# Kernel tuning notes

Hardware: AMD Instinct MI355X
Metric: run time of the kernel (lower is better)

The kernel has to match this reference:

```python
import jax, jax.numpy as jnp
import numpy as np

DIM = 1536; HEADS = 12; HD = DIM // HEADS; FFN = 8960; EPS = 1e-6; T5 = 512
B = 1; F_ = 8; H_ = 18; W_ = 24; S = F_ * H_ * W_; L2 = T5 + 257


def _ln(x, w=None, b=None):
    m = x.mean(-1, keepdims=True)
    v = ((x - m) ** 2).mean(-1, keepdims=True)
    y = (x - m) * jax.lax.rsqrt(v + EPS)
    return y * w + b if w is not None else y


def _rms(x, w):
    return x * jax.lax.rsqrt(jnp.mean(x * x, -1, keepdims=True) + EPS) * w


def _gelu_tanh(z):
    return 0.5 * z * (1.0 + jnp.tanh(0.7978845608028654 * (z + 0.044715 * z * z * z)))


def _rope(x, F, H, W, ang):
    # x: [B,S,n,d]; ang: [1024, d//2] rotation angles (axial 3D RoPE)
    b, s, n, d = x.shape
    c = d // 2
    c1 = c // 3; c0 = c - 2 * c1  # split sizes [c0, c1, c1] over (F,H,W)
    fa = jnp.broadcast_to(ang[:F, :c0][:, None, None, :], (F, H, W, c0))
    ha = jnp.broadcast_to(ang[:H, c0:c0 + c1][None, :, None, :], (F, H, W, c1))
    wa = jnp.broadcast_to(ang[:W, c0 + c1:][None, None, :, :], (F, H, W, c1))
    th = jnp.concatenate([fa, ha, wa], -1).reshape(1, s, 1, c)
    cs, sn = jnp.cos(th), jnp.sin(th)
    xr = x.reshape(b, s, n, c, 2)
    re, im = xr[..., 0], xr[..., 1]
    return jnp.stack([re * cs - im * sn, re * sn + im * cs], -1).reshape(b, s, n, d)


def _attn(q, k, v):
    # dense softmax attention; [B,Lq,n,d] x [B,Lk,n,d]
    s = jnp.einsum('bqnd,bknd->bnqk', q, k) * (1.0 / np.sqrt(q.shape[-1]))
    p = jax.nn.softmax(s, axis=-1)
    return jnp.einsum('bnqk,bknd->bqnd', p, v)


def setup_inputs() -> dict:
    key = jax.random.key(0)
    ks = iter(jax.random.split(key, 64))
    g = lambda shp, sc=0.02: jax.random.normal(next(ks), shp, dtype=jnp.float32) * sc
    inp = {
        'x': jax.random.normal(next(ks), (B, S, DIM), dtype=jnp.float32),
        'e': jax.random.normal(next(ks), (B, 6, DIM), dtype=jnp.float32),
        'context': jax.random.normal(next(ks), (B, L2, DIM), dtype=jnp.float32),
        'freqs': jax.random.uniform(next(ks), (1024, HD // 2), dtype=jnp.float32),
        'modulation': g((1, 6, DIM)),
        'sa_qw': g((DIM, DIM)), 'sa_qb': jnp.zeros((DIM,), jnp.float32),
        'sa_kw': g((DIM, DIM)), 'sa_kb': jnp.zeros((DIM,), jnp.float32),
        'sa_vw': g((DIM, DIM)), 'sa_vb': jnp.zeros((DIM,), jnp.float32),
        'sa_ow': g((DIM, DIM)), 'sa_ob': jnp.zeros((DIM,), jnp.float32),
        'sa_nq': jnp.ones((DIM,), jnp.float32), 'sa_nk': jnp.ones((DIM,), jnp.float32),
        'norm3_w': jnp.ones((DIM,), jnp.float32), 'norm3_b': jnp.zeros((DIM,), jnp.float32),
        'ca_qw': g((DIM, DIM)), 'ca_qb': jnp.zeros((DIM,), jnp.float32),
        'ca_kw': g((DIM, DIM)), 'ca_kb': jnp.zeros((DIM,), jnp.float32),
        'ca_vw': g((DIM, DIM)), 'ca_vb': jnp.zeros((DIM,), jnp.float32),
        'ca_kiw': g((DIM, DIM)), 'ca_kib': jnp.zeros((DIM,), jnp.float32),
        'ca_viw': g((DIM, DIM)), 'ca_vib': jnp.zeros((DIM,), jnp.float32),
        'ca_ow': g((DIM, DIM)), 'ca_ob': jnp.zeros((DIM,), jnp.float32),
        'ca_nq': jnp.ones((DIM,), jnp.float32), 'ca_nk': jnp.ones((DIM,), jnp.float32),
        'ca_nki': jnp.ones((DIM,), jnp.float32),
        'ffn_w1': g((DIM, FFN)), 'ffn_b1': jnp.zeros((FFN,), jnp.float32),
        'ffn_w2': g((FFN, DIM)), 'ffn_b2': jnp.zeros((DIM,), jnp.float32),
        'F': F_, 'H': H_, 'W': W_,
    }
    return inp


def reference(x, e, context, freqs, modulation, sa_qw, sa_qb, sa_kw, sa_kb, sa_vw, sa_vb,
              sa_ow, sa_ob, sa_nq, sa_nk, norm3_w, norm3_b, ca_qw, ca_qb, ca_kw, ca_kb,
              ca_vw, ca_vb, ca_kiw, ca_kib, ca_viw, ca_vib, ca_ow, ca_ob, ca_nq, ca_nk,
              ca_nki, ffn_w1, ffn_b1, ffn_w2, ffn_b2, F, H, W):
    b, s, c = x.shape
    e6 = modulation + e                    # [B,6,C]
    e0, e1, e2, e3, e4, e5 = [e6[:, i:i + 1] for i in range(6)]

    # ---- self attention (with 3D RoPE, qk RMSNorm) ----
    xs = _ln(x) * (1.0 + e1) + e0
    q = _rms(xs @ sa_qw + sa_qb, sa_nq).reshape(b, s, HEADS, HD)
    k = _rms(xs @ sa_kw + sa_kb, sa_nk).reshape(b, s, HEADS, HD)
    v = (xs @ sa_vw + sa_vb).reshape(b, s, HEADS, HD)
    q = _rope(q, F, H, W, freqs)
    k = _rope(k, F, H, W, freqs)
    y = _attn(q, k, v).reshape(b, s, c) @ sa_ow + sa_ob
    x = x + y * e2

    # ---- i2v cross attention: text tokens (last T5) + image tokens (first L2-T5) ----
    xc = _ln(x, norm3_w, norm3_b)
    img_len = context.shape[1] - T5
    ctx_img = context[:, :img_len]
    ctx_txt = context[:, img_len:]
    q = _rms(xc @ ca_qw + ca_qb, ca_nq).reshape(b, s, HEADS, HD)
    k = _rms(ctx_txt @ ca_kw + ca_kb, ca_nk).reshape(b, T5, HEADS, HD)
    v = (ctx_txt @ ca_vw + ca_vb).reshape(b, T5, HEADS, HD)
    ki = _rms(ctx_img @ ca_kiw + ca_kib, ca_nki).reshape(b, img_len, HEADS, HD)
    vi = (ctx_img @ ca_viw + ca_vib).reshape(b, img_len, HEADS, HD)
    a = _attn(q, k, v) + _attn(q, ki, vi)
    x = x + a.reshape(b, s, c) @ ca_ow + ca_ob

    # ---- FFN with adaLN modulation ----
    z = _ln(x) * (1.0 + e4) + e3
    y = _gelu_tanh(z @ ffn_w1 + ffn_b1) @ ffn_w2 + ffn_b2
    x = x + y * e5
    return x
```

## Files before the change

kernel.cpp:

```cpp
#include <hip/hip_runtime.h>
#include <stdint.h>

#define DIM 1536
#define NHEADS 12
#define HD 128
#define FFN 8960
#define SQ 3456
#define T5 512
#define LCTX 769
#define IMG 257
#define IMGP 384
#define EPSL 1e-6f

typedef __bf16 bf16;
typedef __bf16 bf16x8 __attribute__((ext_vector_type(8)));
typedef float f32x4 __attribute__((ext_vector_type(4)));

__device__ inline bf16x8 zero_bf16x8() {
  bf16x8 v;
  for (int i = 0; i < 8; i++) v[i] = (bf16)0.0f;
  return v;
}

__device__ inline void glds16(const bf16* g, bf16* lds) {
  __builtin_amdgcn_global_load_lds(
      (const __attribute__((address_space(1))) void*)g,
      (__attribute__((address_space(3))) void*)lds, 16, 0, 0);
}

__device__ inline bf16x8 rot8(bf16x8 v, int r) {
  union U { bf16x8 b; uint32_t d[4]; };
  U u; u.b = v;
  uint32_t e0 = (r & 4) ? u.d[2] : u.d[0], e1 = (r & 4) ? u.d[3] : u.d[1];
  uint32_t e2 = (r & 4) ? u.d[0] : u.d[2], e3 = (r & 4) ? u.d[1] : u.d[3];
  uint32_t f0 = (r & 2) ? e1 : e0, f1 = (r & 2) ? e2 : e1;
  uint32_t f2 = (r & 2) ? e3 : e2, f3 = (r & 2) ? e0 : e3;
  U o;
  o.d[0] = (r & 1) ? __builtin_amdgcn_alignbit(f1, f0, 16) : f0;
  o.d[1] = (r & 1) ? __builtin_amdgcn_alignbit(f2, f1, 16) : f1;
  o.d[2] = (r & 1) ? __builtin_amdgcn_alignbit(f3, f2, 16) : f2;
  o.d[3] = (r & 1) ? __builtin_amdgcn_alignbit(f0, f3, 16) : f3;
  return o.b;
}


__global__ void prep_small_kernel(const float* __restrict__ modv, const float* __restrict__ e,
                                  float* __restrict__ e6f,
                                  const float* __restrict__ qb, const float* __restrict__ kb,
                                  const float* __restrict__ vb, float* __restrict__ qkvB,
                                  const float* __restrict__ ckb, const float* __restrict__ cvb,
                                  float* __restrict__ kvB,
                                  const float* __restrict__ kib, const float* __restrict__ vib,
                                  float* __restrict__ kivB) {
  int i = blockIdx.x * 256 + threadIdx.x;
  if (i < 6 * DIM) e6f[i] = modv[i] + e[i];
  if (i < DIM) {
    qkvB[i] = qb[i]; qkvB[i + DIM] = kb[i]; qkvB[i + 2 * DIM] = vb[i];
    kvB[i] = ckb[i]; kvB[i + DIM] = cvb[i];
    kivB[i] = kib[i]; kivB[i + DIM] = vib[i];
  }
}

__global__ void prep_ctx_kernel(const float* __restrict__ ctx, bf16* __restrict__ ctxt,
                                bf16* __restrict__ ctxi) {
  int i = blockIdx.x * 256 + threadIdx.x;
  if (i < T5 * DIM) ctxt[i] = (bf16)ctx[(size_t)IMG * DIM + i];
  if (i < IMGP * DIM) {
    int r = i / DIM;
    ctxi[i] = (r < IMG) ? (bf16)ctx[i] : (bf16)0.0f;
  }
}

__global__ void transpose_w3_kernel(const float* __restrict__ W0, const float* __restrict__ W1,
                                    const float* __restrict__ W2, bf16* __restrict__ Wt,
                                    int K, int N) {
  __shared__ float tile[32][33];
  const float* W = blockIdx.z == 0 ? W0 : (blockIdx.z == 1 ? W1 : W2);
  bf16* dst = Wt + (size_t)blockIdx.z * K * N;
  int n0 = blockIdx.x * 32, k0 = blockIdx.y * 32;
  int tx = threadIdx.x, ty = threadIdx.y;
  for (int i = ty; i < 32; i += 8)
    tile[i][tx] = W[(size_t)(k0 + i) * N + n0 + tx];
  __syncthreads();
  for (int i = ty; i < 32; i += 8)
    dst[(size_t)(n0 + i) * K + k0 + tx] = (bf16)tile[tx][i];
}

__device__ inline void block_reduce2(float& s1, float& s2) {
  __shared__ float buf[8];
  for (int off = 32; off; off >>= 1) {
    s1 += __shfl_down(s1, off, 64);
    s2 += __shfl_down(s2, off, 64);
  }
  int w = threadIdx.x >> 6;
  if ((threadIdx.x & 63) == 0) { buf[w] = s1; buf[w + 4] = s2; }
  __syncthreads();
  s1 = buf[0] + buf[1] + buf[2] + buf[3];
  s2 = buf[4] + buf[5] + buf[6] + buf[7];
  __syncthreads();
}

__global__ __launch_bounds__(256) void ln_mod_kernel(
    const float* __restrict__ X, const float* __restrict__ gamma,
    const float* __restrict__ beta, int plus_one, bf16* __restrict__ out) {
  int r = blockIdx.x;
  const float* xr = X + (size_t)r * DIM;
  float v[6], s = 0.f, s2 = 0.f;
  for (int i = 0; i < 6; i++) {
    v[i] = xr[threadIdx.x + i * 256];
    s += v[i]; s2 += v[i] * v[i];
  }
  block_reduce2(s, s2);
  float mean = s * (1.0f / DIM);
  float var = s2 * (1.0f / DIM) - mean * mean;
  float rstd = rsqrtf(var + EPSL);
  float add1 = plus_one ? 1.0f : 0.0f;
  for (int i = 0; i < 6; i++) {
    int c = threadIdx.x + i * 256;
    out[(size_t)r * DIM + c] = (bf16)(((v[i] - mean) * rstd) * (gamma[c] + add1) + beta[c]);
  }
}

__global__ __launch_bounds__(256) void rms_rope_multi_kernel(
    const float* __restrict__ X, int istride, int nsec,
    const float* __restrict__ nw0, const float* __restrict__ nw1,
    int mode0, int mode1, int mode2,
    const float* __restrict__ freqs,
    bf16* __restrict__ o0, bf16* __restrict__ o1, bf16* __restrict__ o2) {
  int sec = blockIdx.y;
  int r = blockIdx.x;
  const float* xr = X + (size_t)r * istride + sec * DIM;
  const float* nw = sec == 0 ? nw0 : nw1;
  bf16* out = (sec == 0 ? o0 : (sec == 1 ? o1 : o2)) + (size_t)r * DIM;
  int mode = sec == 0 ? mode0 : (sec == 1 ? mode1 : mode2);
  float v[6];
  for (int i = 0; i < 6; i++) v[i] = xr[threadIdx.x + i * 256];
  if (mode == 0) {
    for (int i = 0; i < 6; i++) out[threadIdx.x + i * 256] = (bf16)v[i];
    return;
  }
  float s2 = 0.f, dummy = 0.f;
  for (int i = 0; i < 6; i++) s2 += v[i] * v[i];
  block_reduce2(s2, dummy);
  float rms = rsqrtf(s2 * (1.0f / DIM) + EPSL);
  if (mode == 1) {
    for (int i = 0; i < 6; i++) {
      int c = threadIdx.x + i * 256;
      out[c] = (bf16)(v[i] * rms * nw[c]);
    }
  } else {
    int f = r / (18 * 24), rem = r % (18 * 24), hh = rem / 24, ww = rem % 24;
    for (int i = 0; i < 3; i++) {
      int p = threadIdx.x + i * 256;
      int id = p & 63;
      int idx = id < 22 ? f : (id < 43 ? hh : ww);
      float th = freqs[idx * 64 + id];
      float cs = __cosf(th), sn = __sinf(th);
      float re = xr[2 * p] * rms * nw[2 * p];
      float im = xr[2 * p + 1] * rms * nw[2 * p + 1];
      out[2 * p]     = (bf16)(re * cs - im * sn);
      out[2 * p + 1] = (bf16)(re * sn + im * cs);
    }
  }
}

__global__ void ffn2_reduce_kernel(const float* __restrict__ p, const float* __restrict__ b2,
                                   const float* __restrict__ e5, const float* __restrict__ xcur,
                                   float* __restrict__ out) {
  int i = blockIdx.x * 256 + threadIdx.x;
  if (i >= SQ * DIM) return;
  int col = i % DIM;
  out[i] = xcur[i] + (p[i] + p[i + (size_t)SQ * DIM] + b2[col]) * e5[col];
}

template <int BM>
__global__ __launch_bounds__(256) void gemm_db_kernel(
    const bf16* __restrict__ A, const bf16* __restrict__ Wt,
    const float* __restrict__ bias, const float* __restrict__ scalev,
    const float* __restrict__ resid, float* __restrict__ outF,
    bf16* __restrict__ outB, int M, int N, int K, int gelu, int ksplit) {
  constexpr int MI = BM / 32;
  constexpr int NAW = BM / 64;
  __shared__ bf16 As[2][BM * 32];
  __shared__ bf16 Bs[2][128 * 32];
  int tid = threadIdx.x;
  int tm0 = blockIdx.y * BM, tn0 = blockIdx.x * 128;
  int lane = tid & 63, wave = tid >> 6;
  int quad = lane >> 4, l16 = lane & 15;
  int mbase = (wave >> 1) * (BM / 2), nbase = (wave & 1) * 64;
  int lrow = lane >> 2, lcol = (lane & 3) * 8;
  int klen = K / ksplit;
  int kbeg = blockIdx.z * klen;

  const bf16* aP[NAW];
  const bf16* bP[2];
#pragma unroll
  for (int j = 0; j < NAW; j++) {
    int c = wave * NAW + j;
    aP[j] = A + (size_t)(tm0 + c * 16 + lrow) * K + kbeg + lcol;
  }
#pragma unroll
  for (int j = 0; j < 2; j++) {
    int c = wave * 2 + j;
    bP[j] = Wt + (size_t)(tn0 + c * 16 + lrow) * K + kbeg + lcol;
  }

  f32x4 acc[MI][4];
#pragma unroll
  for (int mi = 0; mi < MI; mi++)
    for (int ni = 0; ni < 4; ni++)
      for (int rr = 0; rr < 4; rr++) acc[mi][ni][rr] = 0.0f;

  auto stage = [&](int buf) {
#pragma unroll
    for (int j = 0; j < NAW; j++) {
      glds16(aP[j], &As[buf][(wave * NAW + j) * 512]);
      aP[j] += 32;
    }
#pragma unroll
    for (int j = 0; j < 2; j++) {
      glds16(bP[j], &Bs[buf][(wave * 2 + j) * 512]);
      bP[j] += 32;
    }
  };

  int niter = klen / 32;
  stage(0);
  int cur = 0;
  for (int it = 0; it < niter; it++) {
    __syncthreads();
    if (it + 1 < niter) stage(cur ^ 1);
    bf16x8 af[MI], bfr[4];
#pragma unroll
    for (int mi = 0; mi < MI; mi++)
      af[mi] = *(bf16x8*)&As[cur][(mbase + mi * 16 + l16) * 32 + quad * 8];
#pragma unroll
    for (int ni = 0; ni < 4; ni++)
      bfr[ni] = *(bf16x8*)&Bs[cur][(nbase + ni * 16 + l16) * 32 + quad * 8];
#pragma unroll
    for (int mi = 0; mi < MI; mi++)
#pragma unroll
      for (int ni = 0; ni < 4; ni++)
        acc[mi][ni] = __builtin_amdgcn_mfma_f32_16x16x32_bf16(af[mi], bfr[ni], acc[mi][ni], 0, 0, 0);
    cur ^= 1;
  }

  if (ksplit > 1) {
    float* po = outF + (size_t)blockIdx.z * M * N;
#pragma unroll
    for (int mi = 0; mi < MI; mi++) {
      int rbase = tm0 + mbase + mi * 16 + quad * 4;
#pragma unroll
      for (int ni = 0; ni < 4; ni++) {
        int col = tn0 + nbase + ni * 16 + l16;
        for (int rr = 0; rr < 4; rr++)
          po[(size_t)(rbase + rr) * N + col] = acc[mi][ni][rr];
      }
    }
    return;
  }

#pragma unroll
  for (int mi = 0; mi < MI; mi++) {
    int rbase = tm0 + mbase + mi * 16 + quad * 4;
#pragma unroll
    for (int ni = 0; ni < 4; ni++) {
      int col = tn0 + nbase + ni * 16 + l16;
      float b = bias ? bias[col] : 0.0f;
      float sc = scalev ? scalev[col] : 1.0f;
      for (int rr = 0; rr < 4; rr++) {
        int row = rbase + rr;
        float t = acc[mi][ni][rr] + b;
        if (gelu) {
          float z = t;
          float u = 0.7978845608028654f * (z + 0.044715f * z * z * z);
          t = z / (1.0f + __expf(-2.0f * u));
        }
        t *= sc;
        size_t idx = (size_t)row * N + col;
        if (resid) t += resid[idx];
        if (outF) outF[idx] = t;
        else outB[idx] = (bf16)t;
      }
    }
  }
}

__global__ __launch_bounds__(256) void attn_kernel(
    const bf16* __restrict__ Q, const bf16* __restrict__ Kb, const bf16* __restrict__ Vb,
    float* __restrict__ Opart, float* __restrict__ mlb,
    int L, int kchunk, int zoff) {
  __shared__ bf16 Ks[64][136];
  __shared__ bf16 Vts[128][72];
  __shared__ bf16 Ps[4][16][72];

  int nwg = gridDim.x * gridDim.y * gridDim.z;
  int flat = blockIdx.x + gridDim.x * (blockIdx.y + gridDim.y * blockIdx.z);
  if ((nwg & 7) == 0) flat = (flat & 7) * (nwg >> 3) + (flat >> 3);
  int bx = flat % gridDim.x;
  int rest = flat / gridDim.x;
  int hb = rest % gridDim.y;
  int bz = rest / gridDim.y;

  int tid = threadIdx.x;
  int q0 = bx * 64;
  int zabs = zoff + bz;
  int kbeg = bz * kchunk;
  int kend = min(L, kbeg + kchunk);
  int klen = kend - kbeg;
  int lane = tid & 63, wave = tid >> 6;
  int quad = lane >> 4, l16 = lane & 15;
  int qrow = q0 + wave * 16 + l16;

  bf16x8 qf[4];
#pragma unroll
  for (int c = 0; c < 4; c++)
    qf[c] = *(const bf16x8*)(Q + (size_t)qrow * DIM + hb * HD + c * 32 + quad * 8);

  bf16x8 onesv;
#pragma unroll
  for (int i = 0; i < 8; i++) onesv[i] = (bf16)1.0f;

  f32x4 o[8];
#pragma unroll
  for (int ff = 0; ff < 8; ff++)
    for (int rr = 0; rr < 4; rr++) o[ff][rr] = 0.0f;
  float m_i[4], l_i[4];
#pragma unroll
  for (int r = 0; r < 4; r++) { m_i[r] = -1e30f; l_i[r] = 0.0f; }
  const float sc = 0.08838834764831845f;

  int srow = tid >> 2, scolc = tid & 3;
  int rot = (2 * scolc + (srow & 1)) & 7;
  int nt = (klen + 63) / 64;

  const bf16* kp0 = Kb + (size_t)(kbeg + srow) * DIM + hb * HD + scolc * 8;
  const bf16* vp0 = Vb + (size_t)(kbeg + srow) * DIM + hb * HD + scolc * 8;

  bf16x8 kreg[4], vreg[4];
  if (srow < klen) {
#pragma unroll
    for (int c = 0; c < 4; c++) {
      kreg[c] = *(const bf16x8*)(kp0 + c * 32);
      vreg[c] = *(const bf16x8*)(vp0 + c * 32);
    }
  } else {
#pragma unroll
    for (int c = 0; c < 4; c++) { kreg[c] = zero_bf16x8(); vreg[c] = zero_bf16x8(); }
  }

  for (int kt = 0; kt < nt; kt++) {
    __syncthreads();
#pragma unroll
    for (int c = 0; c < 4; c++)
      *(bf16x8*)&Ks[srow][scolc * 8 + c * 32] = kreg[c];
#pragma unroll
    for (int c = 0; c < 4; c++) {
      bf16x8 rv = rot8(vreg[c], rot);
      int v0 = scolc * 8 + c * 32;
#pragma unroll
      for (int i = 0; i < 8; i++) {
        int jj = (i + rot) & 7;
        Vts[v0 + jj][srow] = rv[i];
      }
    }
    if (kt + 1 < nt) {
      int key = (kt + 1) * 64 + srow;
      const bf16* kp = kp0 + (size_t)(kt + 1) * 64 * DIM;
      const bf16* vp = vp0 + (size_t)(kt + 1) * 64 * DIM;
      if (key < klen) {
#pragma unroll
        for (int c = 0; c < 4; c++) {
          kreg[c] = *(const bf16x8*)(kp + c * 32);
          vreg[c] = *(const bf16x8*)(vp + c * 32);
        }
      } else {
#pragma unroll
        for (int c = 0; c < 4; c++) { kreg[c] = zero_bf16x8(); vreg[c] = zero_bf16x8(); }
      }
    }
    __syncthreads();

    f32x4 sfr[4];
    __builtin_amdgcn_s_setprio(1);
#pragma unroll
    for (int nf = 0; nf < 4; nf++) {
      f32x4 a;
      for (int rr = 0; rr < 4; rr++) a[rr] = 0.0f;
#pragma unroll
      for (int c = 0; c < 4; c++) {
        bf16x8 kf = *(bf16x8*)&Ks[nf * 16 + l16][c * 32 + quad * 8];
        a = __builtin_amdgcn_mfma_f32_16x16x32_bf16(qf[c], kf, a, 0, 0, 0);
      }
      sfr[nf] = a;
    }
    __builtin_amdgcn_s_setprio(0);

#pragma unroll
    for (int nf = 0; nf < 4; nf++) {
      int colg = kt * 64 + nf * 16 + l16;
      bool valid = colg < klen;
#pragma unroll
      for (int r = 0; r < 4; r++)
        sfr[nf][r] = valid ? sfr[nf][r] * sc : -1e30f;
    }

    float lmax[4];
#pragma unroll
    for (int r = 0; r < 4; r++)
      lmax[r] = fmaxf(fmaxf(sfr[0][r], sfr[1][r]), fmaxf(sfr[2][r], sfr[3][r]));
    int ok = (lmax[0] <= m_i[0] + 8.0f) & (lmax[1] <= m_i[1] + 8.0f) &
             (lmax[2] <= m_i[2] + 8.0f) & (lmax[3] <= m_i[3] + 8.0f);
    if (!__all(ok)) {
#pragma unroll
      for (int r = 0; r < 4; r++) {
        float t = lmax[r];
#pragma unroll
        for (int off = 1; off < 16; off <<= 1) t = fmaxf(t, __shfl_xor(t, off, 64));
        float mnew = fmaxf(m_i[r], t);
        float alpha = __expf(m_i[r] - mnew);
        m_i[r] = mnew;
        l_i[r] *= alpha;
#pragma unroll
        for (int ff = 0; ff < 8; ff++) o[ff][r] *= alpha;
      }
    }

#pragma unroll
    for (int r = 0; r < 4; r++) {
      char* prow = (char*)&Ps[wave][quad * 4 + r][0];
      int swzW = ((quad >> 1) & 1) << 5;
#pragma unroll
      for (int nf = 0; nf < 4; nf++) {
        float p = __expf(sfr[nf][r] - m_i[r]);
        *(bf16*)(prow + (((nf * 16 + l16) * 2) ^ swzW)) = (bf16)p;
      }
    }
    int swzR = ((l16 >> 3) & 1) << 5;
    bf16x8 pf[2];
#pragma unroll
    for (int ks = 0; ks < 2; ks++)
      pf[ks] = *(bf16x8*)((char*)&Ps[wave][l16][0] + (((ks * 32 + quad * 8) * 2) ^ swzR));

    __builtin_amdgcn_s_setprio(1);
    f32x4 ld;
    for (int rr = 0; rr < 4; rr++) ld[rr] = 0.0f;
    ld = __builtin_amdgcn_mfma_f32_16x16x32_bf16(pf[0], onesv, ld, 0, 0, 0);
    ld = __builtin_amdgcn_mfma_f32_16x16x32_bf16(pf[1], onesv, ld, 0, 0, 0);
#pragma unroll
    for (int ff = 0; ff < 8; ff++) {
#pragma unroll
      for (int ks = 0; ks < 2; ks++) {
        bf16x8 vf = *(bf16x8*)&Vts[ff * 16 + l16][ks * 32 + quad * 8];
        o[ff] = __builtin_amdgcn_mfma_f32_16x16x32_bf16(pf[ks], vf, o[ff], 0, 0, 0);
      }
    }
    __builtin_amdgcn_s_setprio(0);
#pragma unroll
    for (int r = 0; r < 4; r++) l_i[r] += ld[r];
  }

  float* po = Opart + (size_t)zabs * SQ * DIM;
#pragma unroll
  for (int r = 0; r < 4; r++) {
    float inv = 1.0f / l_i[r];
#pragma unroll
    for (int ff = 0; ff < 8; ff++) o[ff][r] *= inv;
  }
#pragma unroll
  for (int ff = 0; ff < 8; ff++) {
#pragma unroll
    for (int r = 0; r < 4; r++) {
      int row = q0 + wave * 16 + quad * 4 + r;
      int col = hb * HD + ff * 16 + l16;
      po[(size_t)row * DIM + col] = o[ff][r];
    }
  }
  if (l16 == 0) {
#pragma unroll
    for (int r = 0; r < 4; r++) {
      int row = q0 + wave * 16 + quad * 4 + r;
      size_t mi = (((size_t)zabs * NHEADS + hb) * SQ + row) * 2;
      mlb[mi] = m_i[r];
      mlb[mi + 1] = l_i[r];
    }
  }
}

__global__ __launch_bounds__(256) void attn_combine_kernel(
    const float* __restrict__ Op, const float* __restrict__ mlb,
    bf16* __restrict__ out, int nmerge, int addslot) {
  int row = blockIdx.x;
  __shared__ float wsh[3 * NHEADS];
  int t = threadIdx.x;
  if (t < NHEADS) {
    float m[3], l[3];
    for (int z = 0; z < 3; z++) {
      if (z < nmerge) {
        size_t b = (((size_t)z * NHEADS + t) * SQ + row) * 2;
        m[z] = mlb[b]; l[z] = mlb[b + 1];
      } else {
        m[z] = -1e30f; l[z] = 0.0f;
      }
    }
    float M = fmaxf(m[0], fmaxf(m[1], m[2]));
    float w0 = l[0] * __expf(m[0] - M);
    float w1 = l[1] * __expf(m[1] - M);
    float w2 = l[2] * __expf(m[2] - M);
    float inv = 1.0f / (w0 + w1 + w2);
    wsh[t] = w0 * inv;
    wsh[NHEADS + t] = w1 * inv;
    wsh[2 * NHEADS + t] = w2 * inv;
  }
  __syncthreads();
#pragma unroll
  for (int i = 0; i < 6; i++) {
    int c = t + i * 256;
    int h = c >> 7;
    float acc = wsh[h] * Op[((size_t)0 * SQ + row) * DIM + c];
    if (nmerge > 1) acc += wsh[NHEADS + h] * Op[((size_t)1 * SQ + row) * DIM + c];
    if (nmerge > 2) acc += wsh[2 * NHEADS + h] * Op[((size_t)2 * SQ + row) * DIM + c];
    if (addslot >= 0) acc += Op[((size_t)addslot * SQ + row) * DIM + c];
    out[(size_t)row * DIM + c] = (bf16)acc;
  }
}


extern "C" void kernel_launch(void* const* d_in, const int* in_sizes, int n_in,
                              void* d_out, int out_size, void* d_ws, size_t ws_size,
                              hipStream_t stream) {
  const float* x      = (const float*)d_in[0];
  const float* e      = (const float*)d_in[1];
  const float* ctx    = (const float*)d_in[2];
  const float* freqs  = (const float*)d_in[3];
  const float* modv   = (const float*)d_in[4];
  const float* sa_qw  = (const float*)d_in[5];
  const float* sa_qb  = (const float*)d_in[6];
  const float* sa_kw  = (const float*)d_in[7];
  const float* sa_kb  = (const float*)d_in[8];
  const float* sa_vw  = (const float*)d_in[9];
  const float* sa_vb  = (const float*)d_in[10];
  const float* sa_ow  = (const float*)d_in[11];
  const float* sa_ob  = (const float*)d_in[12];
  const float* sa_nq  = (const float*)d_in[13];
  const float* sa_nk  = (const float*)d_in[14];
  const float* norm3w = (const float*)d_in[15];
  const float* norm3b = (const float*)d_in[16];
  const float* ca_qw  = (const float*)d_in[17];
  const float* ca_qb  = (const float*)d_in[18];
  const float* ca_kw  = (const float*)d_in[19];
  const float* ca_kb  = (const float*)d_in[20];
  const float* ca_vw  = (const float*)d_in[21];
  const float* ca_vb  = (const float*)d_in[22];
  const float* ca_kiw = (const float*)d_in[23];
  const float* ca_kib = (const float*)d_in[24];
  const float* ca_viw = (const float*)d_in[25];
  const float* ca_vib = (const float*)d_in[26];
  const float* ca_ow  = (const float*)d_in[27];
  const float* ca_ob  = (const float*)d_in[28];
  const float* ca_nq  = (const float*)d_in[29];
  const float* ca_nk  = (const float*)d_in[30];
  const float* ca_nki = (const float*)d_in[31];
  const float* ffn_w1 = (const float*)d_in[32];
  const float* ffn_b1 = (const float*)d_in[33];
  const float* ffn_w2 = (const float*)d_in[34];
  const float* ffn_b2 = (const float*)d_in[35];

  char* ws = (char*)d_ws;
  size_t off = 0;
  auto alloc = [&](size_t bytes) -> void* {
    void* p = ws + off;
    off += (bytes + 255) & ~(size_t)255;
    return p;
  };
  float* e6f   = (float*)alloc((size_t)6 * DIM * 4);
  bf16* act_bf = (bf16*)alloc((size_t)SQ * DIM * 2);
  bf16* q_bf   = (bf16*)alloc((size_t)SQ * DIM * 2);
  bf16* k_bf   = (bf16*)alloc((size_t)SQ * DIM * 2);
  bf16* v_bf   = (bf16*)alloc((size_t)SQ * DIM * 2);
  char* big0   = (char*)alloc((size_t)SQ * 3 * DIM * 4);
  float* xcur  = (float*)alloc((size_t)SQ * DIM * 4);
  bf16* wbig   = (bf16*)alloc((size_t)FFN * DIM * 2);
  bf16* wsm    = (bf16*)alloc((size_t)3 * DIM * DIM * 2);
  bf16* ctxt_bf = (bf16*)alloc((size_t)T5 * DIM * 2);
  bf16* ctxi_bf = (bf16*)alloc((size_t)IMGP * DIM * 2);
  float* ctxkvF = (float*)alloc((size_t)T5 * 2 * DIM * 4);
  float* ctxkivF = (float*)alloc((size_t)IMGP * 2 * DIM * 4);
  bf16* kt_bf  = (bf16*)alloc((size_t)T5 * DIM * 2);
  bf16* vt_bf  = (bf16*)alloc((size_t)T5 * DIM * 2);
  bf16* ki_bf  = (bf16*)alloc((size_t)IMGP * DIM * 2);
  bf16* vi_bf  = (bf16*)alloc((size_t)IMGP * DIM * 2);
  float* qkvB  = (float*)alloc((size_t)3 * DIM * 4);
  float* kvB   = (float*)alloc((size_t)2 * DIM * 4);
  float* kivB  = (float*)alloc((size_t)2 * DIM * 4);
  float* mlbuf = (float*)alloc((size_t)3 * NHEADS * SQ * 2 * 4);

  float* qkvF = (float*)big0;
  float* projf = (float*)big0;
  float* opart = (float*)big0;
  bf16* y1 = (bf16*)big0;
  float* pbuf = (float*)act_bf;

  const float* e0 = e6f;
  const float* e1 = e6f + DIM;
  const float* e2 = e6f + 2 * DIM;
  const float* e3 = e6f + 3 * DIM;
  const float* e4 = e6f + 4 * DIM;
  const float* e5 = e6f + 5 * DIM;

  dim3 tblk(32, 8);

  prep_small_kernel<<<(6 * DIM + 255) / 256, 256, 0, stream>>>(
      modv, e, e6f, sa_qb, sa_kb, sa_vb, qkvB, ca_kb, ca_vb, kvB, ca_kib, ca_vib, kivB);

  ln_mod_kernel<<<SQ, 256, 0, stream>>>(x, e1, e0, 1, act_bf);

  transpose_w3_kernel<<<dim3(48, 48, 3), tblk, 0, stream>>>(sa_qw, sa_kw, sa_vw, wbig, DIM, DIM);
  gemm_db_kernel<128><<<dim3(3 * DIM / 128, SQ / 128), 256, 0, stream>>>(
      act_bf, wbig, qkvB, nullptr, nullptr, qkvF, nullptr, SQ, 3 * DIM, DIM, 0, 1);
  rms_rope_multi_kernel<<<dim3(SQ, 3), 256, 0, stream>>>(
      qkvF, 3 * DIM, 3, sa_nq, sa_nk, 2, 2, 0, freqs, q_bf, k_bf, v_bf);

  attn_kernel<<<dim3(SQ / 64, NHEADS, 3), 256, 0, stream>>>(
      q_bf, k_bf, v_bf, opart, mlbuf, SQ, SQ / 3, 0);
  attn_combine_kernel<<<SQ, 256, 0, stream>>>(opart, mlbuf, act_bf, 3, -1);

  transpose_w3_kernel<<<dim3(48, 48, 1), tblk, 0, stream>>>(sa_ow, nullptr, nullptr, wsm, DIM, DIM);
  gemm_db_kernel<64><<<dim3(DIM / 128, SQ / 64), 256, 0, stream>>>(
      act_bf, wsm, sa_ob, e2, x, xcur, nullptr, SQ, DIM, DIM, 0, 1);

  ln_mod_kernel<<<SQ, 256, 0, stream>>>(xcur, norm3w, norm3b, 0, act_bf);

  transpose_w3_kernel<<<dim3(48, 48, 1), tblk, 0, stream>>>(ca_qw, nullptr, nullptr, wsm, DIM, DIM);
  gemm_db_kernel<64><<<dim3(DIM / 128, SQ / 64), 256, 0, stream>>>(
      act_bf, wsm, ca_qb, nullptr, nullptr, projf, nullptr, SQ, DIM, DIM, 0, 1);
  rms_rope_multi_kernel<<<dim3(SQ, 1), 256, 0, stream>>>(
      projf, DIM, 1, ca_nq, nullptr, 1, 0, 0, freqs, q_bf, nullptr, nullptr);

  prep_ctx_kernel<<<(T5 * DIM + 255) / 256, 256, 0, stream>>>(ctx, ctxt_bf, ctxi_bf);

  transpose_w3_kernel<<<dim3(48, 48, 2), tblk, 0, stream>>>(ca_kw, ca_vw, nullptr, wsm, DIM, DIM);
  gemm_db_kernel<64><<<dim3(2 * DIM / 128, T5 / 64), 256, 0, stream>>>(
      ctxt_bf, wsm, kvB, nullptr, nullptr, ctxkvF, nullptr, T5, 2 * DIM, DIM, 0, 1);
  rms_rope_multi_kernel<<<dim3(T5, 2), 256, 0, stream>>>(
      ctxkvF, 2 * DIM, 2, ca_nk, nullptr, 1, 0, 0, freqs, kt_bf, vt_bf, nullptr);

  transpose_w3_kernel<<<dim3(48, 48, 2), tblk, 0, stream>>>(ca_kiw, ca_viw, nullptr, wsm, DIM, DIM);
  gemm_db_kernel<64><<<dim3(2 * DIM / 128, IMGP / 64), 256, 0, stream>>>(
      ctxi_bf, wsm, kivB, nullptr, nullptr, ctxkivF, nullptr, IMGP, 2 * DIM, DIM, 0, 1);
  rms_rope_multi_kernel<<<dim3(IMGP, 2), 256, 0, stream>>>(
      ctxkivF, 2 * DIM, 2, ca_nki, nullptr, 1, 0, 0, freqs, ki_bf, vi_bf, nullptr);

  attn_kernel<<<dim3(SQ / 64, NHEADS, 2), 256, 0, stream>>>(
      q_bf, kt_bf, vt_bf, opart, mlbuf, T5, T5 / 2, 0);
  attn_kernel<<<dim3(SQ / 64, NHEADS, 1), 256, 0, stream>>>(
      q_bf, ki_bf, vi_bf, opart, mlbuf, IMG, IMG, 2);
  attn_combine_kernel<<<SQ, 256, 0, stream>>>(opart, mlbuf, act_bf, 2, 2);

  transpose_w3_kernel<<<dim3(48, 48, 1), tblk, 0, stream>>>(ca_ow, nullptr, nullptr, wsm, DIM, DIM);
  gemm_db_kernel<64><<<dim3(DIM / 128, SQ / 64), 256, 0, stream>>>(
      act_bf, wsm, ca_ob, nullptr, xcur, xcur, nullptr, SQ, DIM, DIM, 0, 1);

  ln_mod_kernel<<<SQ, 256, 0, stream>>>(xcur, e4, e3, 1, act_bf);

  transpose_w3_kernel<<<dim3(FFN / 32, 48, 1), tblk, 0, stream>>>(ffn_w1, nullptr, nullptr, wbig, DIM, FFN);
  gemm_db_kernel<128><<<dim3(FFN / 128, SQ / 128), 256, 0, stream>>>(
      act_bf, wbig, ffn_b1, nullptr, nullptr, nullptr, y1, SQ, FFN, DIM, 1, 1);

  transpose_w3_kernel<<<dim3(48, FFN / 32, 1), tblk, 0, stream>>>(ffn_w2, nullptr, nullptr, wbig, FFN, DIM);
  gemm_db_kernel<128><<<dim3(DIM / 128, SQ / 128, 2), 256, 0, stream>>>(
      y1, wbig, nullptr, nullptr, nullptr, pbuf, nullptr, SQ, DIM, FFN, 0, 2);
  ffn2_reduce_kernel<<<(SQ * DIM + 255) / 256, 256, 0, stream>>>(
      pbuf, ffn_b2, e5, xcur, (float*)d_out);
}
```

Before: 1.244 ms.

## Fold softmax scale and log2e into Q, use exp2, merge cross-attn launches

Q is pre-scaled by 1/sqrt(d)·log2(e) inside the RMS/RoPE kernel, so the attention kernel uses exp2f and no longer multiplies scores by the scale. The key-padding mask now runs only on the final partial tile, and the rescale threshold is widened to match log2 units. The two cross-attention launches (text and image keys) become one launch that selects the K/V source by z-index. This removes per-score multiplies and one kernel launch, at the cost of a small bf16 rounding difference in Q.

```diff
diff --git a/kernel.cpp b/kernel.cpp
--- a/kernel.cpp
+++ b/kernel.cpp
@@ -124,7 +124,7 @@
 __global__ __launch_bounds__(256) void rms_rope_multi_kernel(
     const float* __restrict__ X, int istride, int nsec,
     const float* __restrict__ nw0, const float* __restrict__ nw1,
-    int mode0, int mode1, int mode2,
+    int mode0, int mode1, int mode2, float s0scale,
     const float* __restrict__ freqs,
     bf16* __restrict__ o0, bf16* __restrict__ o1, bf16* __restrict__ o2) {
   int sec = blockIdx.y;
@@ -143,6 +143,7 @@
   for (int i = 0; i < 6; i++) s2 += v[i] * v[i];
   block_reduce2(s2, dummy);
   float rms = rsqrtf(s2 * (1.0f / DIM) + EPSL);
+  if (sec == 0) rms *= s0scale;
   if (mode == 1) {
     for (int i = 0; i < 6; i++) {
       int c = threadIdx.x + i * 256;
@@ -288,8 +289,9 @@
 
 __global__ __launch_bounds__(256) void attn_kernel(
     const bf16* __restrict__ Q, const bf16* __restrict__ Kb, const bf16* __restrict__ Vb,
+    const bf16* __restrict__ Kb2, const bf16* __restrict__ Vb2,
     float* __restrict__ Opart, float* __restrict__ mlb,
-    int L, int kchunk, int zoff) {
+    int L, int kchunk, int zsplit1, int Lsec, int kchunk2) {
   __shared__ bf16 Ks[64][136];
   __shared__ bf16 Vts[128][72];
   __shared__ bf16 Ps[4][16][72];
@@ -304,10 +306,16 @@
 
   int tid = threadIdx.x;
   int q0 = bx * 64;
-  int zabs = zoff + bz;
-  int kbeg = bz * kchunk;
-  int kend = min(L, kbeg + kchunk);
+  int sec = bz >= zsplit1;
+  int bzl = sec ? bz - zsplit1 : bz;
+  const bf16* Kp = sec ? Kb2 : Kb;
+  const bf16* Vp = sec ? Vb2 : Vb;
+  int Lv = sec ? Lsec : L;
+  int kch = sec ? kchunk2 : kchunk;
+  int kbeg = bzl * kch;
+  int kend = min(Lv, kbeg + kch);
   int klen = kend - kbeg;
+  int zabs = bz;
   int lane = tid & 63, wave = tid >> 6;
   int quad = lane >> 4, l16 = lane & 15;
   int qrow = q0 + wave * 16 + l16;
@@ -328,14 +336,14 @@
   float m_i[4], l_i[4];
 #pragma unroll
   for (int r = 0; r < 4; r++) { m_i[r] = -1e30f; l_i[r] = 0.0f; }
-  const float sc = 0.08838834764831845f;
 
   int srow = tid >> 2, scolc = tid & 3;
   int rot = (2 * scolc + (srow & 1)) & 7;
   int nt = (klen + 63) / 64;
-
-  const bf16* kp0 = Kb + (size_t)(kbeg + srow) * DIM + hb * HD + scolc * 8;
-  const bf16* vp0 = Vb + (size_t)(kbeg + srow) * DIM + hb * HD + scolc * 8;
+  int tail = (klen & 63) != 0;
+
+  const bf16* kp0 = Kp + (size_t)(kbeg + srow) * DIM + hb * HD + scolc * 8;
+  const bf16* vp0 = Vp + (size_t)(kbeg + srow) * DIM + hb * HD + scolc * 8;
 
   bf16x8 kreg[4], vreg[4];
   if (srow < klen) {
@@ -396,21 +404,23 @@
     }
     __builtin_amdgcn_s_setprio(0);
 
-#pragma unroll
-    for (int nf = 0; nf < 4; nf++) {
-      int colg = kt * 64 + nf * 16 + l16;
-      bool valid = colg < klen;
-#pragma unroll
-      for (int r = 0; r < 4; r++)
-        sfr[nf][r] = valid ? sfr[nf][r] * sc : -1e30f;
+    if (tail && kt == nt - 1) {
+#pragma unroll
+      for (int nf = 0; nf < 4; nf++) {
+        int colg = kt * 64 + nf * 16 + l16;
+        bool valid = colg < klen;
+#pragma unroll
+        for (int r = 0; r < 4; r++)
+          sfr[nf][r] = valid ? sfr[nf][r] : -1e30f;
+      }
     }
 
     float lmax[4];
 #pragma unroll
     for (int r = 0; r < 4; r++)
       lmax[r] = fmaxf(fmaxf(sfr[0][r], sfr[1][r]), fmaxf(sfr[2][r], sfr[3][r]));
-    int ok = (lmax[0] <= m_i[0] + 8.0f) & (lmax[1] <= m_i[1] + 8.0f) &
-             (lmax[2] <= m_i[2] + 8.0f) & (lmax[3] <= m_i[3] + 8.0f);
+    int ok = (lmax[0] <= m_i[0] + 11.54f) & (lmax[1] <= m_i[1] + 11.54f) &
+             (lmax[2] <= m_i[2] + 11.54f) & (lmax[3] <= m_i[3] + 11.54f);
     if (!__all(ok)) {
 #pragma unroll
       for (int r = 0; r < 4; r++) {
@@ -418,7 +428,7 @@
 #pragma unroll
         for (int off = 1; off < 16; off <<= 1) t = fmaxf(t, __shfl_xor(t, off, 64));
         float mnew = fmaxf(m_i[r], t);
-        float alpha = __expf(m_i[r] - mnew);
+        float alpha = exp2f(m_i[r] - mnew);
         m_i[r] = mnew;
         l_i[r] *= alpha;
 #pragma unroll
@@ -432,7 +442,7 @@
       int swzW = ((quad >> 1) & 1) << 5;
 #pragma unroll
       for (int nf = 0; nf < 4; nf++) {
-        float p = __expf(sfr[nf][r] - m_i[r]);
+        float p = exp2f(sfr[nf][r] - m_i[r]);
         *(bf16*)(prow + (((nf * 16 + l16) * 2) ^ swzW)) = (bf16)p;
       }
     }
@@ -504,9 +514,9 @@
       }
     }
     float M = fmaxf(m[0], fmaxf(m[1], m[2]));
-    float w0 = l[0] * __expf(m[0] - M);
-    float w1 = l[1] * __expf(m[1] - M);
-    float w2 = l[2] * __expf(m[2] - M);
+    float w0 = l[0] * exp2f(m[0] - M);
+    float w1 = l[1] * exp2f(m[1] - M);
+    float w2 = l[2] * exp2f(m[2] - M);
     float inv = 1.0f / (w0 + w1 + w2);
     wsh[t] = w0 * inv;
     wsh[NHEADS + t] = w1 * inv;
@@ -608,6 +618,8 @@
   const float* e4 = e6f + 4 * DIM;
   const float* e5 = e6f + 5 * DIM;
 
+  const float SCL2 = 0.12751744f;
+
   dim3 tblk(32, 8);
 
   prep_small_kernel<<<(6 * DIM + 255) / 256, 256, 0, stream>>>(
@@ -619,10 +631,10 @@
   gemm_db_kernel<128><<<dim3(3 * DIM / 128, SQ / 128), 256, 0, stream>>>(
       act_bf, wbig, qkvB, nullptr, nullptr, qkvF, nullptr, SQ, 3 * DIM, DIM, 0, 1);
   rms_rope_multi_kernel<<<dim3(SQ, 3), 256, 0, stream>>>(
-      qkvF, 3 * DIM, 3, sa_nq, sa_nk, 2, 2, 0, freqs, q_bf, k_bf, v_bf);
+      qkvF, 3 * DIM, 3, sa_nq, sa_nk, 2, 2, 0, SCL2, freqs, q_bf, k_bf, v_bf);
 
   attn_kernel<<<dim3(SQ / 64, NHEADS, 3), 256, 0, stream>>>(
-      q_bf, k_bf, v_bf, opart, mlbuf, SQ, SQ / 3, 0);
+      q_bf, k_bf, v_bf, k_bf, v_bf, opart, mlbuf, SQ, SQ / 3, 3, SQ, SQ / 3);
   attn_combine_kernel<<<SQ, 256, 0, stream>>>(opart, mlbuf, act_bf, 3, -1);
 
   transpose_w3_kernel<<<dim3(48, 48, 1), tblk, 0, stream>>>(sa_ow, nullptr, nullptr, wsm, DIM, DIM);
@@ -635,7 +647,7 @@
   gemm_db_kernel<64><<<dim3(DIM / 128, SQ / 64), 256, 0, stream>>>(
       act_bf, wsm, ca_qb, nullptr, nullptr, projf, nullptr, SQ, DIM, DIM, 0, 1);
   rms_rope_multi_kernel<<<dim3(SQ, 1), 256, 0, stream>>>(
-      projf, DIM, 1, ca_nq, nullptr, 1, 0, 0, freqs, q_bf, nullptr, nullptr);
+      projf, DIM, 1, ca_nq, nullptr, 1, 0, 0, SCL2, freqs, q_bf, nullptr, nullptr);
 
   prep_ctx_kernel<<<(T5 * DIM + 255) / 256, 256, 0, stream>>>(ctx, ctxt_bf, ctxi_bf);
 
@@ -643,18 +655,16 @@
   gemm_db_kernel<64><<<dim3(2 * DIM / 128, T5 / 64), 256, 0, stream>>>(
       ctxt_bf, wsm, kvB, nullptr, nullptr, ctxkvF, nullptr, T5, 2 * DIM, DIM, 0, 1);
   rms_rope_multi_kernel<<<dim3(T5, 2), 256, 0, stream>>>(
-      ctxkvF, 2 * DIM, 2, ca_nk, nullptr, 1, 0, 0, freqs, kt_bf, vt_bf, nullptr);
+      ctxkvF, 2 * DIM, 2, ca_nk, nullptr, 1, 0, 0, 1.0f, freqs, kt_bf, vt_bf, nullptr);
 
   transpose_w3_kernel<<<dim3(48, 48, 2), tblk, 0, stream>>>(ca_kiw, ca_viw, nullptr, wsm, DIM, DIM);
   gemm_db_kernel<64><<<dim3(2 * DIM / 128, IMGP / 64), 256, 0, stream>>>(
       ctxi_bf, wsm, kivB, nullptr, nullptr, ctxkivF, nullptr, IMGP, 2 * DIM, DIM, 0, 1);
   rms_rope_multi_kernel<<<dim3(IMGP, 2), 256, 0, stream>>>(
-      ctxkivF, 2 * DIM, 2, ca_nki, nullptr, 1, 0, 0, freqs, ki_bf, vi_bf, nullptr);
-
-  attn_kernel<<<dim3(SQ / 64, NHEADS, 2), 256, 0, stream>>>(
-      q_bf, kt_bf, vt_bf, opart, mlbuf, T5, T5 / 2, 0);
-  attn_kernel<<<dim3(SQ / 64, NHEADS, 1), 256, 0, stream>>>(
-      q_bf, ki_bf, vi_bf, opart, mlbuf, IMG, IMG, 2);
+      ctxkivF, 2 * DIM, 2, ca_nki, nullptr, 1, 0, 0, 1.0f, freqs, ki_bf, vi_bf, nullptr);
+
+  attn_kernel<<<dim3(SQ / 64, NHEADS, 3), 256, 0, stream>>>(
+      q_bf, kt_bf, vt_bf, ki_bf, vi_bf, opart, mlbuf, T5, T5 / 2, 2, IMG, IMG);
   attn_combine_kernel<<<SQ, 256, 0, stream>>>(opart, mlbuf, act_bf, 2, 2);
 
   transpose_w3_kernel<<<dim3(48, 48, 1), tblk, 0, stream>>>(ca_ow, nullptr, nullptr, wsm, DIM, DIM);
```

Result: no change. 1.244 ms (+0.0%).
